# Optimization experiments

Hardware: AMD Instinct MI355X
Metric: run time of the kernel (lower is better)

Reference implementation:

```python
import jax, jax.numpy as jnp
import numpy as np

NS, NH, NL, NP, E = 2, 8, 4, 4, 256
HD = E // NH  # 32


def grid_sample_zeros(img, grid):
    """torch.F.grid_sample(mode='bilinear', padding_mode='zeros', align_corners=False).
    img: [B, C, Hs, Ws]; grid: [B, Hg, Wg, 2] with (x, y) in [-1, 1]. Returns [B, C, Hg, Wg]."""
    B, C, Hs, Ws = img.shape
    gx = (grid[..., 0] + 1.0) * (Ws * 0.5) - 0.5  # pixel-space x
    gy = (grid[..., 1] + 1.0) * (Hs * 0.5) - 0.5  # pixel-space y
    x0 = jnp.floor(gx)
    y0 = jnp.floor(gy)
    x1, y1 = x0 + 1.0, y0 + 1.0
    wx1 = gx - x0
    wx0 = 1.0 - wx1
    wy1 = gy - y0
    wy0 = 1.0 - wy1
    imgf = img.reshape(B, C, Hs * Ws)

    def gather(ix, iy):
        valid = (ix >= 0) & (ix < Ws) & (iy >= 0) & (iy < Hs)
        ixc = jnp.clip(ix, 0, Ws - 1).astype(jnp.int32)
        iyc = jnp.clip(iy, 0, Hs - 1).astype(jnp.int32)
        flat = (iyc * Ws + ixc).reshape(B, 1, -1)
        vals = jnp.take_along_axis(imgf, flat, axis=2).reshape(B, C, *ix.shape[1:])
        return vals * valid[:, None].astype(img.dtype)

    return (gather(x0, y0) * (wx0 * wy0)[:, None]
            + gather(x1, y0) * (wx1 * wy0)[:, None]
            + gather(x0, y1) * (wx0 * wy1)[:, None]
            + gather(x1, y1) * (wx1 * wy1)[:, None])


def setup_inputs() -> dict:
    key = jax.random.key(0)
    ks = jax.random.split(key, 10)
    bs, Q = 2048, NL * NP  # num_query forced to num_levels*num_points = 16
    f = jnp.float32
    s = 1.0 / np.sqrt(E)
    return {
        "query": jax.random.normal(ks[0], (bs, Q, E), f),
        "key_hist": jax.random.normal(ks[1], (bs, Q, E), f),
        "value_hist": jax.random.normal(ks[2], (bs, Q, E), f),
        "reference_points": jax.random.uniform(ks[3], (bs, Q, NL, 2), f),
        "spatial_shapes": jnp.full((NL, 2), 2, dtype=jnp.int32),  # each level 2x2, sum HW = 16
        "Wq": jax.random.normal(ks[4], (E, E), f) * s, "bq": jnp.zeros((E,), f),
        "Wk": jax.random.normal(ks[5], (E, E), f) * s, "bk": jnp.zeros((E,), f),
        "Wv": jax.random.normal(ks[6], (E, E), f) * s, "bv": jnp.zeros((E,), f),
        "Woff": jax.random.normal(ks[7], (E, NH * NL * NP * 2), f) * (0.01 * s), "boff": jnp.zeros((NH * NL * NP * 2,), f),
        "Wout": jax.random.normal(ks[8], (E, E), f) * s, "bout": jnp.zeros((E,), f),
    }


def reference(query, key_hist, value_hist, reference_points, spatial_shapes,
              Wq, bq, Wk, bk, Wv, bv, Woff, boff, Wout, bout):
    bs, Q, _ = query.shape
    B = bs * NS
    residual = query

    # torch cat(dim=1)+view interleaves the two sequences per batch: index 2b -> query, 2b+1 -> hist
    queries = jnp.repeat(query, NS, axis=0)                              # [B, Q, E]
    keys = jnp.stack([query, key_hist], axis=1).reshape(B, Q, E)
    values = jnp.stack([query, value_hist], axis=1).reshape(B, Q, E)
    rp = jnp.repeat(reference_points, NS, axis=0)                        # [B, Q, NL, 2] (both copies identical)

    qh = (queries @ Wq + bq).reshape(B, Q, NH, HD)
    kh = (keys @ Wk + bk).reshape(B, Q, NH, HD)
    vh = (values @ Wv + bv).reshape(B, Q, NH, HD)

    attn = jax.nn.softmax(jnp.einsum('bqhd,bkhd->bqhk', qh, kh), axis=-1)
    attn = attn.reshape(B, Q, NH, NL, NP)

    offsets = (queries @ Woff + boff).reshape(B, Q, NH, NL, NP, 2)
    norm = jnp.stack([spatial_shapes[:, 1], spatial_shapes[:, 0]], axis=-1).astype(query.dtype)  # (W, H)
    loc = rp[:, :, None, :, None, :] + offsets / norm[None, None, None, :, None, :]
    grid = 2.0 * loc - 1.0                                               # [B, Q, NH, NL, NP, 2]

    ss = np.asarray(spatial_shapes)                                      # static level shapes
    attw = attn.transpose(0, 2, 1, 3, 4).reshape(B * NH, Q, NL, NP)      # [BH, Q, NL, NP]
    acc = jnp.zeros((B * NH, HD, Q), dtype=query.dtype)
    start = 0
    for l in range(NL):
        H_, W_ = int(ss[l, 0]), int(ss[l, 1])
        hw = H_ * W_
        v_l = vh[:, start:start + hw].transpose(0, 2, 3, 1).reshape(B * NH, HD, H_, W_)
        g_l = grid[:, :, :, l].transpose(0, 2, 1, 3, 4).reshape(B * NH, Q, NP, 2)
        s_l = grid_sample_zeros(v_l, g_l)                                # [BH, HD, Q, NP]
        acc = acc + jnp.sum(s_l * attw[:, None, :, l, :], axis=-1)       # weighted reduce over points
        start += hw

    out = acc.reshape(B, E, Q).transpose(0, 2, 1)                        # [B, Q, E]
    out = out.reshape(bs, NS, Q, E).mean(axis=1)                         # mean over the two sequences
    return out @ Wout + bout + residual                                  # dropout is identity in eval
```

## Files before the change

### kernel.cpp

```cpp
#include <hip/hip_runtime.h>

typedef float  f32x4  __attribute__((ext_vector_type(4)));
typedef __bf16 bf16x8 __attribute__((ext_vector_type(8)));
typedef __bf16 bf16x4 __attribute__((ext_vector_type(4)));

__device__ __forceinline__ bf16x8 cvt8(float4 a, float4 b) {
    bf16x8 r;
    r[0] = (__bf16)a.x; r[1] = (__bf16)a.y; r[2] = (__bf16)a.z; r[3] = (__bf16)a.w;
    r[4] = (__bf16)b.x; r[5] = (__bf16)b.y; r[6] = (__bf16)b.z; r[7] = (__bf16)b.w;
    return r;
}

#define OF_OFF 524288
#define PV_OFF (1u << 20)

__global__ void wprep(const float* __restrict__ Wq, const float* __restrict__ Wk,
                      const float* __restrict__ Wv, const float* __restrict__ Woff,
                      const float* __restrict__ Wout, __bf16* __restrict__ ws) {
    int id = blockIdx.x * 256 + threadIdx.x;
    if (id < 262144) {
        int tile = id >> 9, e = id & 511;
        int lane = e >> 3, j = e & 7;
        int kt = tile & 7, nh = (tile >> 3) & 1, mat = (tile >> 4) & 3, h = tile >> 6;
        int k = kt * 32 + (lane >> 4) * 8 + j;
        int col = h * 32 + nh * 16 + (lane & 15);
        const float* W = (mat == 0) ? Wq : (mat == 1) ? Wk : (mat == 2) ? Wv : Woff;
        ws[id] = (__bf16)W[k * 256 + col];
    } else {
        int i = id - 262144;
        int tile = i >> 9, e = i & 511;
        int lane = e >> 3, j = e & 7;
        int kt = tile & 7, nt = tile >> 3;
        int k = kt * 32 + (lane >> 4) * 8 + j;
        int col = nt * 16 + (lane & 15);
        ws[262144 + i] = (__bf16)Wout[k * 256 + col];
    }
}

__launch_bounds__(512, 4)
__global__ void tsa_one(const float* __restrict__ query, const float* __restrict__ keyh,
                        const float* __restrict__ valh, const float* __restrict__ refpts,
                        unsigned char* __restrict__ wsw,
                        const float* __restrict__ bq, const float* __restrict__ bk,
                        const float* __restrict__ bv, const float* __restrict__ boff,
                        const float* __restrict__ bout, float* __restrict__ out, int b0)
{
    __shared__ __attribute__((aligned(16))) unsigned char uni[16384];
    __shared__ __attribute__((aligned(16))) unsigned char scr_all[24576];
    __shared__ __attribute__((aligned(16))) unsigned char vfr[32768];
    const int t = threadIdx.x;
    const int lane = t & 63, w = t >> 6, l15 = lane & 15, lhi = lane >> 4;
    const int p = w >> 1;
    const int role = w & 1;
    const long b = (long)b0 + (long)blockIdx.x * 4 + p;
    unsigned char* scrp = scr_all + p * 6144;
    unsigned char* vfrp = vfr + p * 8192;
    __bf16* pvg = (__bf16*)(wsw + PV_OFF) + ((long)blockIdx.x * 4 + p) * 4096;

    bf16x8 afr[8];
    {
        const float* s0 = (role ? keyh : query) + b * 4096 + l15 * 256;
        #pragma unroll
        for (int kt = 0; kt < 8; ++kt) {
            int o = kt * 32 + lhi * 8;
            afr[kt] = cvt8(*(const float4*)(s0 + o), *(const float4*)(s0 + o + 4));
        }
        if (role) {
            const float* s1 = valh + b * 4096 + l15 * 256;
            #pragma unroll
            for (int kt = 0; kt < 8; ++kt) {
                int o = kt * 32 + lhi * 8;
                *(bf16x8*)(vfrp + kt * 1024 + lane * 16) =
                    cvt8(*(const float4*)(s1 + o), *(const float4*)(s1 + o + 4));
            }
        }
    }
    const f32x4 z = (f32x4){0.f, 0.f, 0.f, 0.f};
    float2 rp = *(const float2*)(refpts + b * 128 + l15 * 8 + lhi * 2);
    __syncthreads();

    for (int h = 0; h < 8; ++h) {
        #pragma unroll 2
        for (int nh = 0; nh < 2; ++nh) {
            f32x4 acc[4];
            #pragma unroll
            for (int i = 0; i < 4; ++i) acc[i] = z;
            #pragma unroll 2
            for (int half = 0; half < 2; ++half) {
                __syncthreads();
                #pragma unroll
                for (int it = 0; it < 2; ++it) {
                    int u = t + it * 512;
                    int f = u >> 6;
                    int kt = (half << 2) + (f & 3);
                    const void* src = (const void*)(wsw +
                        ((((h * 4 + (f >> 2)) * 2 + nh) * 8 + kt) << 10) + (u & 63) * 16);
                    __builtin_amdgcn_global_load_lds(
                        (const __attribute__((address_space(1))) unsigned int*)src,
                        (__attribute__((address_space(3))) unsigned int*)(uni + u * 16),
                        16, 0, 0);
                }
                __syncthreads();
                #pragma unroll
                for (int ktl = 0; ktl < 4; ++ktl) {
                    int kt = (half << 2) + ktl;
                    const unsigned char* bb = uni + ktl * 1024 + lane * 16;
                    bf16x8 b_k = *(const bf16x8*)(bb + 4096);
                    bf16x8 b_v = *(const bf16x8*)(bb + 8192);
                    if (!role) {
                        bf16x8 b_q = *(const bf16x8*)(bb);
                        bf16x8 b_o = *(const bf16x8*)(bb + 12288);
                        acc[0] = __builtin_amdgcn_mfma_f32_16x16x32_bf16(afr[kt], b_q, acc[0], 0, 0, 0);
                        acc[1] = __builtin_amdgcn_mfma_f32_16x16x32_bf16(afr[kt], b_k, acc[1], 0, 0, 0);
                        acc[2] = __builtin_amdgcn_mfma_f32_16x16x32_bf16(afr[kt], b_v, acc[2], 0, 0, 0);
                        acc[3] = __builtin_amdgcn_mfma_f32_16x16x32_bf16(afr[kt], b_o, acc[3], 0, 0, 0);
                    } else {
                        bf16x8 av = *(const bf16x8*)(vfrp + kt * 1024 + lane * 16);
                        acc[0] = __builtin_amdgcn_mfma_f32_16x16x32_bf16(afr[kt], b_k, acc[0], 0, 0, 0);
                        acc[1] = __builtin_amdgcn_mfma_f32_16x16x32_bf16(av,      b_v, acc[1], 0, 0, 0);
                    }
                }
            }
            {
                int dcol = nh * 16 + l15;
                int gcol = h * 32 + dcol;
                if (!role) {
                    float bqv = bq[gcol], bkv = bk[gcol], bvv = bv[gcol], bov = boff[gcol];
                    #pragma unroll
                    for (int r = 0; r < 4; ++r) {
                        int row = lhi * 4 + r;
                        *(__bf16*)(scrp + row * 64 + dcol * 2)        = (__bf16)(acc[0][r] + bqv);
                        *(__bf16*)(scrp + 1024 + row * 64 + dcol * 2) = (__bf16)(acc[1][r] + bkv);
                        *(__bf16*)(scrp + 3072 + dcol * 64 + row * 2) = (__bf16)(acc[2][r] + bvv);
                        *(__bf16*)(scrp + 5120 + row * 64 + dcol * 2) = (__bf16)(acc[3][r] + bov);
                    }
                } else {
                    float bkv = bk[gcol], bvv = bv[gcol];
                    #pragma unroll
                    for (int r = 0; r < 4; ++r) {
                        int row = lhi * 4 + r;
                        *(__bf16*)(scrp + 2048 + row * 64 + dcol * 2)      = (__bf16)(acc[0][r] + bkv);
                        *(__bf16*)(scrp + 3072 + dcol * 64 + 32 + row * 2) = (__bf16)(acc[1][r] + bvv);
                    }
                }
            }
        }
        __syncthreads();

        bf16x8 qf = *(const bf16x8*)(scrp + l15 * 64 + lhi * 16);
        bf16x8 kf = *(const bf16x8*)(scrp + 1024 + role * 1024 + l15 * 64 + lhi * 16);
        f32x4 S = __builtin_amdgcn_mfma_f32_16x16x32_bf16(kf, qf, z, 0, 0, 0);
        float pr4[4];
        {
            float m = fmaxf(fmaxf(S[0], S[1]), fmaxf(S[2], S[3]));
            m = fmaxf(m, __shfl_xor(m, 16)); m = fmaxf(m, __shfl_xor(m, 32));
            float s = 0.f;
            #pragma unroll
            for (int r = 0; r < 4; ++r) { pr4[r] = __expf(S[r] - m); s += pr4[r]; }
            s += __shfl_xor(s, 16); s += __shfl_xor(s, 32);
            float inv = 1.f / s;
            #pragma unroll
            for (int r = 0; r < 4; ++r) pr4[r] *= inv;
        }

        {
            bf16x8 off8 = *(const bf16x8*)(scrp + 5120 + l15 * 64 + lhi * 16);
            float w4[4] = {0.f, 0.f, 0.f, 0.f};
            #pragma unroll
            for (int pp = 0; pp < 4; ++pp) {
                float gx = 2.f * rp.x + (float)off8[2 * pp]     - 0.5f;
                float gy = 2.f * rp.y + (float)off8[2 * pp + 1] - 0.5f;
                float tx0 = fmaxf(0.f, 1.f - fabsf(gx));
                float tx1 = fmaxf(0.f, 1.f - fabsf(gx - 1.f));
                float ty0 = fmaxf(0.f, 1.f - fabsf(gy));
                float ty1 = fmaxf(0.f, 1.f - fabsf(gy - 1.f));
                w4[0] += tx0 * ty0 * pr4[pp]; w4[1] += tx1 * ty0 * pr4[pp];
                w4[2] += tx0 * ty1 * pr4[pp]; w4[3] += tx1 * ty1 * pr4[pp];
            }
            *(bf16x4*)(scrp + 1024 + role * 1024 + l15 * 64 + lhi * 8) =
                (bf16x4){(__bf16)w4[0], (__bf16)w4[1], (__bf16)w4[2], (__bf16)w4[3]};
        }
        __syncthreads();

        if (role) {
            bf16x8 aW  = *(const bf16x8*)(scrp + 1024 + (lhi >> 1) * 1024 + l15 * 64 + (lhi & 1) * 16);
            bf16x8 vf0 = *(const bf16x8*)(scrp + 3072 + l15 * 64 + lhi * 16);
            bf16x8 vf1 = *(const bf16x8*)(scrp + 3072 + (16 + l15) * 64 + lhi * 16);
            f32x4 c0 = __builtin_amdgcn_mfma_f32_16x16x32_bf16(aW, vf0, z, 0, 0, 0);
            f32x4 c1 = __builtin_amdgcn_mfma_f32_16x16x32_bf16(aW, vf1, z, 0, 0, 0);
            #pragma unroll
            for (int r = 0; r < 4; ++r) {
                int qq = lhi * 4 + r;
                *(__bf16*)(scrp + qq * 64 + l15 * 2)        = (__bf16)(0.5f * c0[r]);
                *(__bf16*)(scrp + qq * 64 + (16 + l15) * 2) = (__bf16)(0.5f * c1[r]);
            }
            bf16x8 pvfrag = *(const bf16x8*)(scrp + l15 * 64 + lhi * 16);
            *(bf16x8*)(pvg + h * 512 + lane * 8) = pvfrag;
        }
    }

    __syncthreads();

    {
        bf16x8 pv[8];
        #pragma unroll
        for (int kt = 0; kt < 8; ++kt)
            pv[kt] = *(const bf16x8*)(pvg + kt * 512 + lane * 8);
        for (int qd = 0; qd < 4; ++qd) {
            f32x4 o2[2];
            o2[0] = z; o2[1] = z;
            #pragma unroll
            for (int kt = 0; kt < 8; ++kt) {
                #pragma unroll
                for (int j = 0; j < 2; ++j) {
                    int ntl = role * 2 + j;
                    bf16x8 bfr = *(const bf16x8*)(wsw + OF_OFF + qd * 32768 +
                                                  (ntl * 8 + kt) * 1024 + lane * 16);
                    o2[j] = __builtin_amdgcn_mfma_f32_16x16x32_bf16(pv[kt], bfr, o2[j], 0, 0, 0);
                }
            }
            #pragma unroll
            for (int j = 0; j < 2; ++j) {
                int ntl = role * 2 + j;
                int col = (qd * 4 + ntl) * 16 + l15;
                float bo = bout[col];
                #pragma unroll
                for (int r = 0; r < 4; ++r) {
                    int qq = lhi * 4 + r;
                    long idx = b * 4096 + qq * 256 + col;
                    out[idx] = o2[j][r] + bo + query[idx];
                }
            }
        }
    }
}

extern "C" void kernel_launch(void* const* d_in, const int* in_sizes, int n_in,
                              void* d_out, int out_size, void* d_ws, size_t ws_size,
                              hipStream_t stream) {
    const float* query      = (const float*)d_in[0];
    const float* key_hist   = (const float*)d_in[1];
    const float* value_hist = (const float*)d_in[2];
    const float* refpts     = (const float*)d_in[3];
    const float* Wq   = (const float*)d_in[5];
    const float* bq   = (const float*)d_in[6];
    const float* Wk   = (const float*)d_in[7];
    const float* bk   = (const float*)d_in[8];
    const float* Wv   = (const float*)d_in[9];
    const float* bv   = (const float*)d_in[10];
    const float* Woff = (const float*)d_in[11];
    const float* boff = (const float*)d_in[12];
    const float* Wout = (const float*)d_in[13];
    const float* bout = (const float*)d_in[14];
    float* outp = (float*)d_out;

    const int bs = in_sizes[0] / 4096;
    wprep<<<1280, 256, 0, stream>>>(Wq, Wk, Wv, Woff, Wout, (__bf16*)d_ws);

    long avail = (long)ws_size - (long)PV_OFF;
    int CB = bs;
    if (avail < (long)bs * 8192) {
        CB = (int)(avail / 8192) & ~3;
        if (CB < 4) CB = 4;
    }
    for (int b0 = 0; b0 < bs; b0 += CB) {
        int nb = (bs - b0 < CB ? bs - b0 : CB) / 4;
        tsa_one<<<nb, 512, 0, stream>>>(query, key_hist, value_hist, refpts,
                                        (unsigned char*)d_ws,
                                        bq, bk, bv, boff, bout, outp, b0);
    }
}
```

Measured before the change: 87.15 us.

## Switch projections to 32x32 MFMA over batch pairs with prefetched weight staging

Restructures the fused Q/K/V/offset projection so each group of four waves computes two batch elements at once (32 rows) with 32x32x16 MFMAs. Each wave now owns one operand/matrix role instead of repeating the weight fragments per batch. The weight staging buffer is doubled to hold a full head half. The first half of the next head is prefetched into LDS while the attention/softmax step runs, and the separate value-fragment LDS buffer is removed. Register pressure rises (16 A fragments, two 16-wide accumulators), so launch bounds drop from 4 to 3 blocks per CU, trading occupancy for better MFMA shape and fewer weight re-reads.

```diff
diff --git a/kernel.cpp b/kernel.cpp
--- a/kernel.cpp
+++ b/kernel.cpp
@@ -1,6 +1,7 @@
 #include <hip/hip_runtime.h>
 
 typedef float  f32x4  __attribute__((ext_vector_type(4)));
+typedef float  f32x16 __attribute__((ext_vector_type(16)));
 typedef __bf16 bf16x8 __attribute__((ext_vector_type(8)));
 typedef __bf16 bf16x4 __attribute__((ext_vector_type(4)));
 
@@ -21,9 +22,9 @@
     if (id < 262144) {
         int tile = id >> 9, e = id & 511;
         int lane = e >> 3, j = e & 7;
-        int kt = tile & 7, nh = (tile >> 3) & 1, mat = (tile >> 4) & 3, h = tile >> 6;
-        int k = kt * 32 + (lane >> 4) * 8 + j;
-        int col = h * 32 + nh * 16 + (lane & 15);
+        int kt = tile & 15, mat = (tile >> 4) & 3, h = tile >> 6;
+        int k = kt * 16 + ((lane >> 5) << 3) + j;
+        int col = h * 32 + (lane & 31);
         const float* W = (mat == 0) ? Wq : (mat == 1) ? Wk : (mat == 2) ? Wv : Woff;
         ws[id] = (__bf16)W[k * 256 + col];
     } else {
@@ -37,7 +38,23 @@
     }
 }
 
-__launch_bounds__(512, 4)
+__device__ __forceinline__ void stage32(const unsigned char* wsw, int h, int half,
+                                        unsigned char* uni, int t) {
+    #pragma unroll
+    for (int it = 0; it < 4; ++it) {
+        int u = t + it * 512;
+        int f = u >> 6;
+        int kt = half * 8 + (f & 7);
+        const void* src = (const void*)(wsw +
+            ((((h * 4 + (f >> 3)) * 16) + kt) << 10) + (u & 63) * 16);
+        __builtin_amdgcn_global_load_lds(
+            (const __attribute__((address_space(1))) unsigned int*)src,
+            (__attribute__((address_space(3))) unsigned int*)(uni + u * 16),
+            16, 0, 0);
+    }
+}
+
+__launch_bounds__(512, 3)
 __global__ void tsa_one(const float* __restrict__ query, const float* __restrict__ keyh,
                         const float* __restrict__ valh, const float* __restrict__ refpts,
                         unsigned char* __restrict__ wsw,
@@ -45,110 +62,96 @@
                         const float* __restrict__ bv, const float* __restrict__ boff,
                         const float* __restrict__ bout, float* __restrict__ out, int b0)
 {
-    __shared__ __attribute__((aligned(16))) unsigned char uni[16384];
+    __shared__ __attribute__((aligned(16))) unsigned char uni[32768];
     __shared__ __attribute__((aligned(16))) unsigned char scr_all[24576];
-    __shared__ __attribute__((aligned(16))) unsigned char vfr[32768];
     const int t = threadIdx.x;
     const int lane = t & 63, w = t >> 6, l15 = lane & 15, lhi = lane >> 4;
-    const int p = w >> 1;
-    const int role = w & 1;
-    const long b = (long)b0 + (long)blockIdx.x * 4 + p;
-    unsigned char* scrp = scr_all + p * 6144;
-    unsigned char* vfrp = vfr + p * 8192;
-    __bf16* pvg = (__bf16*)(wsw + PV_OFF) + ((long)blockIdx.x * 4 + p) * 4096;
-
-    bf16x8 afr[8];
+    const int P = w >> 2, sub = w & 3;
+    const int pa = w >> 1, role = w & 1;
+    const long bpair = (long)b0 + (long)blockIdx.x * 4 + P * 2;
+    const long bT    = (long)b0 + (long)blockIdx.x * 4 + pa;
+    unsigned char* scrT = scr_all + pa * 6144;
+    __bf16* pvg = (__bf16*)(wsw + PV_OFF) + ((long)blockIdx.x * 4 + pa) * 4096;
+
+    stage32(wsw, 0, 0, uni, t);
+
+    bf16x8 afr[16];
     {
-        const float* s0 = (role ? keyh : query) + b * 4096 + l15 * 256;
+        const float* Asrc = (sub <= 1) ? query : (sub == 2 ? keyh : valh);
+        const float* ap = Asrc + bpair * 4096 + (lane & 31) * 256 + ((lane >> 5) << 3);
         #pragma unroll
-        for (int kt = 0; kt < 8; ++kt) {
-            int o = kt * 32 + lhi * 8;
-            afr[kt] = cvt8(*(const float4*)(s0 + o), *(const float4*)(s0 + o + 4));
-        }
-        if (role) {
-            const float* s1 = valh + b * 4096 + l15 * 256;
-            #pragma unroll
-            for (int kt = 0; kt < 8; ++kt) {
-                int o = kt * 32 + lhi * 8;
-                *(bf16x8*)(vfrp + kt * 1024 + lane * 16) =
-                    cvt8(*(const float4*)(s1 + o), *(const float4*)(s1 + o + 4));
-            }
-        }
+        for (int kt = 0; kt < 16; ++kt)
+            afr[kt] = cvt8(*(const float4*)(ap + kt * 16), *(const float4*)(ap + kt * 16 + 4));
     }
     const f32x4 z = (f32x4){0.f, 0.f, 0.f, 0.f};
-    float2 rp = *(const float2*)(refpts + b * 128 + l15 * 8 + lhi * 2);
+    float2 rp = *(const float2*)(refpts + bT * 128 + l15 * 8 + lhi * 2);
     __syncthreads();
 
     for (int h = 0; h < 8; ++h) {
+        const int colv = lane & 31;
+        float biasX, biasY = 0.f;
+        if (sub == 0)      { biasX = bq[h * 32 + colv]; biasY = boff[h * 32 + colv]; }
+        else if (sub == 1) { biasX = bk[h * 32 + colv]; biasY = bv[h * 32 + colv]; }
+        else if (sub == 2) { biasX = bk[h * 32 + colv]; }
+        else               { biasX = bv[h * 32 + colv]; }
+
+        f32x16 accX = {0,0,0,0,0,0,0,0,0,0,0,0,0,0,0,0};
+        f32x16 accY = {0,0,0,0,0,0,0,0,0,0,0,0,0,0,0,0};
+
         #pragma unroll 2
-        for (int nh = 0; nh < 2; ++nh) {
-            f32x4 acc[4];
-            #pragma unroll
-            for (int i = 0; i < 4; ++i) acc[i] = z;
-            #pragma unroll 2
-            for (int half = 0; half < 2; ++half) {
+        for (int half = 0; half < 2; ++half) {
+            if (half == 1) {
                 __syncthreads();
-                #pragma unroll
-                for (int it = 0; it < 2; ++it) {
-                    int u = t + it * 512;
-                    int f = u >> 6;
-                    int kt = (half << 2) + (f & 3);
-                    const void* src = (const void*)(wsw +
-                        ((((h * 4 + (f >> 2)) * 2 + nh) * 8 + kt) << 10) + (u & 63) * 16);
-                    __builtin_amdgcn_global_load_lds(
-                        (const __attribute__((address_space(1))) unsigned int*)src,
-                        (__attribute__((address_space(3))) unsigned int*)(uni + u * 16),
-                        16, 0, 0);
+                stage32(wsw, h, 1, uni, t);
+                __syncthreads();
+            }
+            #pragma unroll
+            for (int kt2 = 0; kt2 < 8; ++kt2) {
+                const int kt = half * 8 + kt2;
+                const unsigned char* base = uni + kt2 * 1024 + lane * 16;
+                if (sub == 0) {
+                    bf16x8 bqf = *(const bf16x8*)(base);
+                    bf16x8 bof = *(const bf16x8*)(base + 24576);
+                    accX = __builtin_amdgcn_mfma_f32_32x32x16_bf16(afr[kt], bqf, accX, 0, 0, 0);
+                    accY = __builtin_amdgcn_mfma_f32_32x32x16_bf16(afr[kt], bof, accY, 0, 0, 0);
+                } else if (sub == 1) {
+                    bf16x8 bkf = *(const bf16x8*)(base + 8192);
+                    bf16x8 bvf = *(const bf16x8*)(base + 16384);
+                    accX = __builtin_amdgcn_mfma_f32_32x32x16_bf16(afr[kt], bkf, accX, 0, 0, 0);
+                    accY = __builtin_amdgcn_mfma_f32_32x32x16_bf16(afr[kt], bvf, accY, 0, 0, 0);
+                } else if (sub == 2) {
+                    bf16x8 bkf = *(const bf16x8*)(base + 8192);
+                    accX = __builtin_amdgcn_mfma_f32_32x32x16_bf16(afr[kt], bkf, accX, 0, 0, 0);
+                } else {
+                    bf16x8 bvf = *(const bf16x8*)(base + 16384);
+                    accX = __builtin_amdgcn_mfma_f32_32x32x16_bf16(afr[kt], bvf, accX, 0, 0, 0);
                 }
-                __syncthreads();
-                #pragma unroll
-                for (int ktl = 0; ktl < 4; ++ktl) {
-                    int kt = (half << 2) + ktl;
-                    const unsigned char* bb = uni + ktl * 1024 + lane * 16;
-                    bf16x8 b_k = *(const bf16x8*)(bb + 4096);
-                    bf16x8 b_v = *(const bf16x8*)(bb + 8192);
-                    if (!role) {
-                        bf16x8 b_q = *(const bf16x8*)(bb);
-                        bf16x8 b_o = *(const bf16x8*)(bb + 12288);
-                        acc[0] = __builtin_amdgcn_mfma_f32_16x16x32_bf16(afr[kt], b_q, acc[0], 0, 0, 0);
-                        acc[1] = __builtin_amdgcn_mfma_f32_16x16x32_bf16(afr[kt], b_k, acc[1], 0, 0, 0);
-                        acc[2] = __builtin_amdgcn_mfma_f32_16x16x32_bf16(afr[kt], b_v, acc[2], 0, 0, 0);
-                        acc[3] = __builtin_amdgcn_mfma_f32_16x16x32_bf16(afr[kt], b_o, acc[3], 0, 0, 0);
-                    } else {
-                        bf16x8 av = *(const bf16x8*)(vfrp + kt * 1024 + lane * 16);
-                        acc[0] = __builtin_amdgcn_mfma_f32_16x16x32_bf16(afr[kt], b_k, acc[0], 0, 0, 0);
-                        acc[1] = __builtin_amdgcn_mfma_f32_16x16x32_bf16(av,      b_v, acc[1], 0, 0, 0);
-                    }
-                }
-            }
-            {
-                int dcol = nh * 16 + l15;
-                int gcol = h * 32 + dcol;
-                if (!role) {
-                    float bqv = bq[gcol], bkv = bk[gcol], bvv = bv[gcol], bov = boff[gcol];
-                    #pragma unroll
-                    for (int r = 0; r < 4; ++r) {
-                        int row = lhi * 4 + r;
-                        *(__bf16*)(scrp + row * 64 + dcol * 2)        = (__bf16)(acc[0][r] + bqv);
-                        *(__bf16*)(scrp + 1024 + row * 64 + dcol * 2) = (__bf16)(acc[1][r] + bkv);
-                        *(__bf16*)(scrp + 3072 + dcol * 64 + row * 2) = (__bf16)(acc[2][r] + bvv);
-                        *(__bf16*)(scrp + 5120 + row * 64 + dcol * 2) = (__bf16)(acc[3][r] + bov);
-                    }
-                } else {
-                    float bkv = bk[gcol], bvv = bv[gcol];
-                    #pragma unroll
-                    for (int r = 0; r < 4; ++r) {
-                        int row = lhi * 4 + r;
-                        *(__bf16*)(scrp + 2048 + row * 64 + dcol * 2)      = (__bf16)(acc[0][r] + bkv);
-                        *(__bf16*)(scrp + 3072 + dcol * 64 + 32 + row * 2) = (__bf16)(acc[1][r] + bvv);
-                    }
-                }
+            }
+        }
+
+        #pragma unroll
+        for (int r = 0; r < 16; ++r) {
+            const int row = (r & 3) + ((r >> 2) << 3) + ((lane >> 5) << 2);
+            const int q = row & 15;
+            unsigned char* sb = scr_all + (P * 2 + (row >> 4)) * 6144;
+            if (sub == 0) {
+                *(__bf16*)(sb + q * 64 + colv * 2)        = (__bf16)(accX[r] + biasX);
+                *(__bf16*)(sb + 5120 + q * 64 + colv * 2) = (__bf16)(accY[r] + biasY);
+            } else if (sub == 1) {
+                *(__bf16*)(sb + 1024 + q * 64 + colv * 2) = (__bf16)(accX[r] + biasX);
+                *(__bf16*)(sb + 3072 + colv * 64 + q * 2) = (__bf16)(accY[r] + biasY);
+            } else if (sub == 2) {
+                *(__bf16*)(sb + 2048 + q * 64 + colv * 2) = (__bf16)(accX[r] + biasX);
+            } else {
+                *(__bf16*)(sb + 3072 + colv * 64 + 32 + q * 2) = (__bf16)(accX[r] + biasX);
             }
         }
         __syncthreads();
 
-        bf16x8 qf = *(const bf16x8*)(scrp + l15 * 64 + lhi * 16);
-        bf16x8 kf = *(const bf16x8*)(scrp + 1024 + role * 1024 + l15 * 64 + lhi * 16);
+        if (h < 7) stage32(wsw, h + 1, 0, uni, t);
+
+        bf16x8 qf = *(const bf16x8*)(scrT + l15 * 64 + lhi * 16);
+        bf16x8 kf = *(const bf16x8*)(scrT + 1024 + role * 1024 + l15 * 64 + lhi * 16);
         f32x4 S = __builtin_amdgcn_mfma_f32_16x16x32_bf16(kf, qf, z, 0, 0, 0);
         float pr4[4];
         {
@@ -164,7 +167,7 @@
         }
 
         {
-            bf16x8 off8 = *(const bf16x8*)(scrp + 5120 + l15 * 64 + lhi * 16);
+            bf16x8 off8 = *(const bf16x8*)(scrT + 5120 + l15 * 64 + lhi * 16);
             float w4[4] = {0.f, 0.f, 0.f, 0.f};
             #pragma unroll
             for (int pp = 0; pp < 4; ++pp) {
@@ -177,24 +180,24 @@
                 w4[0] += tx0 * ty0 * pr4[pp]; w4[1] += tx1 * ty0 * pr4[pp];
                 w4[2] += tx0 * ty1 * pr4[pp]; w4[3] += tx1 * ty1 * pr4[pp];
             }
-            *(bf16x4*)(scrp + 1024 + role * 1024 + l15 * 64 + lhi * 8) =
+            *(bf16x4*)(scrT + 1024 + role * 1024 + l15 * 64 + lhi * 8) =
                 (bf16x4){(__bf16)w4[0], (__bf16)w4[1], (__bf16)w4[2], (__bf16)w4[3]};
         }
         __syncthreads();
 
         if (role) {
-            bf16x8 aW  = *(const bf16x8*)(scrp + 1024 + (lhi >> 1) * 1024 + l15 * 64 + (lhi & 1) * 16);
-            bf16x8 vf0 = *(const bf16x8*)(scrp + 3072 + l15 * 64 + lhi * 16);
-            bf16x8 vf1 = *(const bf16x8*)(scrp + 3072 + (16 + l15) * 64 + lhi * 16);
+            bf16x8 aW  = *(const bf16x8*)(scrT + 1024 + (lhi >> 1) * 1024 + l15 * 64 + (lhi & 1) * 16);
+            bf16x8 vf0 = *(const bf16x8*)(scrT + 3072 + l15 * 64 + lhi * 16);
+            bf16x8 vf1 = *(const bf16x8*)(scrT + 3072 + (16 + l15) * 64 + lhi * 16);
             f32x4 c0 = __builtin_amdgcn_mfma_f32_16x16x32_bf16(aW, vf0, z, 0, 0, 0);
             f32x4 c1 = __builtin_amdgcn_mfma_f32_16x16x32_bf16(aW, vf1, z, 0, 0, 0);
             #pragma unroll
             for (int r = 0; r < 4; ++r) {
                 int qq = lhi * 4 + r;
-                *(__bf16*)(scrp + qq * 64 + l15 * 2)        = (__bf16)(0.5f * c0[r]);
-                *(__bf16*)(scrp + qq * 64 + (16 + l15) * 2) = (__bf16)(0.5f * c1[r]);
-            }
-            bf16x8 pvfrag = *(const bf16x8*)(scrp + l15 * 64 + lhi * 16);
+                *(__bf16*)(scrT + qq * 64 + l15 * 2)        = (__bf16)(0.5f * c0[r]);
+                *(__bf16*)(scrT + qq * 64 + (16 + l15) * 2) = (__bf16)(0.5f * c1[r]);
+            }
+            bf16x8 pvfrag = *(const bf16x8*)(scrT + l15 * 64 + lhi * 16);
             *(bf16x8*)(pvg + h * 512 + lane * 8) = pvfrag;
         }
     }
@@ -227,7 +230,7 @@
                 #pragma unroll
                 for (int r = 0; r < 4; ++r) {
                     int qq = lhi * 4 + r;
-                    long idx = b * 4096 + qq * 256 + col;
+                    long idx = bT * 4096 + qq * 256 + col;
                     out[idx] = o2[j][r] + bo + query[idx];
                 }
             }
```

Measured after the change: 152.2 us. 1.75x slower.
